# Performance work log

Hardware: AMD Instinct MI355X
Metric: run time of the kernel (lower is better)

## Reference

```python
import jax, jax.numpy as jnp
import numpy as np

DIM, HEAD_DIM, NUM_HEAD, RP_DIM = 1024, 64, 16, 256
B, N = 2, 4096
EPS_KERNEL = 1e-4


def _orthogonal_projection(nb_rows, nb_cols, rng):
    # gaussian_orthogonal_random_matrix with scaling=0 (performer-pytorch)
    blocks = []
    full = nb_rows // nb_cols
    for _ in range(full):
        q, _ = np.linalg.qr(rng.standard_normal((nb_cols, nb_cols)))
        blocks.append(q.T)
    rem = nb_rows - full * nb_cols
    if rem > 0:
        q, _ = np.linalg.qr(rng.standard_normal((nb_cols, nb_cols)))
        blocks.append(q.T[:rem])
    mat = np.concatenate(blocks, axis=0)
    multiplier = np.linalg.norm(rng.standard_normal((nb_rows, nb_cols)), axis=1)
    return (multiplier[:, None] * mat).astype(np.float32)


def setup_inputs() -> dict:
    key = jax.random.key(0)
    ks = jax.random.split(key, 10)
    s = (1.0 / np.sqrt(DIM)).astype(np.float32)
    inp = {
        'X': jax.random.normal(ks[0], (B, N, DIM), jnp.float32),
        'mask': jnp.ones((B, N), jnp.float32),
        'W_q': jax.random.normal(ks[1], (DIM, DIM), jnp.float32) * s,
        'b_q': jnp.zeros((DIM,), jnp.float32),
        'W_k': jax.random.normal(ks[2], (DIM, DIM), jnp.float32) * s,
        'b_k': jnp.zeros((DIM,), jnp.float32),
        'W_v': jax.random.normal(ks[3], (DIM, DIM), jnp.float32) * s,
        'b_v': jnp.zeros((DIM,), jnp.float32),
        'W_ff': jax.random.normal(ks[4], (DIM, DIM), jnp.float32) * s,
        'b_ff': jnp.zeros((DIM,), jnp.float32),
        'proj': jnp.asarray(_orthogonal_projection(RP_DIM, HEAD_DIM, np.random.default_rng(0))),
    }
    return inp


def _softmax_kernel(data, proj, is_query):
    # FAVOR+ positive random features (performer-pytorch softmax_kernel)
    d = data.shape[-1]
    normalizer = d ** -0.25
    ratio = proj.shape[0] ** -0.5
    data_dash = jnp.einsum('bhnd,jd->bhnj', normalizer * data, proj)
    diag_data = jnp.sum(data * data, axis=-1, keepdims=True) * 0.5 * (normalizer ** 2)
    if is_query:
        m = jnp.max(data_dash, axis=-1, keepdims=True)
    else:
        m = jnp.max(data_dash, axis=(-1, -2), keepdims=True)
    return ratio * (jnp.exp(data_dash - diag_data - m) + EPS_KERNEL)


def _split_heads(x):
    b, n, _ = x.shape
    return x.reshape(b, n, NUM_HEAD, HEAD_DIM).transpose(0, 2, 1, 3)


def reference(X, mask, W_q, b_q, W_k, b_k, W_v, b_v, W_ff, b_ff, proj):
    Q = _split_heads(X @ W_q.T + b_q)  # [B,H,N,D]
    K = _split_heads(X @ W_k.T + b_k)
    V = _split_heads(X @ W_v.T + b_v)
    scale = HEAD_DIM ** -0.25  # 1/sqrt(sqrt(head_dim)) applied in PerformerAttention.forward
    m = mask[:, None, :, None]
    qp = _softmax_kernel(Q * scale, proj, is_query=True)   # [B,H,N,R]
    kp = _softmax_kernel(K * scale * m, proj, is_query=False)
    Vm = V * m
    # non-causal linear attention
    k_sum = jnp.sum(kp, axis=-2)                                  # [B,H,R]
    D_inv = 1.0 / jnp.einsum('bhnr,bhr->bhn', qp, k_sum)          # [B,H,N]
    context = jnp.einsum('bhnr,bhne->bhre', kp, Vm)               # [B,H,R,D]
    attn = jnp.einsum('bhre,bhnr,bhn->bhne', context, qp, D_inv)  # [B,H,N,D]
    attn = attn.transpose(0, 2, 1, 3).reshape(X.shape[0], X.shape[1], NUM_HEAD * HEAD_DIM)
    return attn @ W_ff.T + b_ff
```

## Files before the change

### kernel.cpp

```cpp
#include <hip/hip_runtime.h>
#include <math.h>

typedef unsigned short u16;
typedef short bf16x8 __attribute__((ext_vector_type(8)));
typedef float f32x4 __attribute__((ext_vector_type(4)));
typedef u16 u16x4 __attribute__((ext_vector_type(4)));

#define RATIO 0.0625f
#define EPSK 1e-4f
#define LOG2E 1.44269504f

__device__ __forceinline__ float bf2f(u16 u) {
  return __uint_as_float(((unsigned)u) << 16);
}
__device__ __forceinline__ u16 f2bf(float f) {
  unsigned x = __float_as_uint(f);
  x = x + 0x7fffu + ((x >> 16) & 1u);
  return (u16)(x >> 16);
}
__device__ __forceinline__ unsigned cvtpk(float a, float b) {
  unsigned d;
  asm("v_cvt_pk_bf16_f32 %0, %1, %2" : "=v"(d) : "v"(a), "v"(b));
  return d;
}

using as1v = __attribute__((address_space(1))) void;
using as3v = __attribute__((address_space(3))) void;
__device__ __forceinline__ void gl_lds16(const void* g, void* l) {
  __builtin_amdgcn_global_load_lds((as1v*)g, (as3v*)l, 16, 0, 0);
}

__global__ __launch_bounds__(256) void cvt_all(
    const float* __restrict__ X, const float* __restrict__ Wq, const float* __restrict__ Wk,
    const float* __restrict__ Wv, const float* __restrict__ Wff, const float* __restrict__ proj,
    u16* __restrict__ Xbf, u16* __restrict__ Wqkv, u16* __restrict__ Wffb, u16* __restrict__ Pbf) {
  long bid = blockIdx.x;
  const float* src;
  u16* dst;
  long off;
  float sc = 1.f;
  if (bid < 8192) { src = X; dst = Xbf; off = bid; }
  else if (bid < 9216) { src = Wq; dst = Wqkv; off = bid - 8192; }
  else if (bid < 10240) { src = Wk; dst = Wqkv + 1048576; off = bid - 9216; }
  else if (bid < 11264) { src = Wv; dst = Wqkv + 2097152; off = bid - 10240; }
  else if (bid < 12288) { src = Wff; dst = Wffb; off = bid - 11264; }
  else { src = proj; dst = Pbf; off = bid - 12288; sc = 0.125f; }
  long i = (off * 256 + threadIdx.x) * 4;
  f32x4 v = *(const f32x4*)(src + i);
  u16x4 o;
#pragma unroll
  for (int j = 0; j < 4; ++j) o[j] = f2bf(v[j] * sc);
  *(u16x4*)(dst + i) = o;
}

template <int EPI, int NB>
__global__ __launch_bounds__(512, 1) void gemmring(
    const u16* __restrict__ A, const u16* __restrict__ Bw,
    const float* __restrict__ bq, const float* __restrict__ bk,
    const float* __restrict__ bv, const float* __restrict__ mask,
    u16* __restrict__ Q, u16* __restrict__ Kb, u16* __restrict__ Vt,
    float* __restrict__ Of, const float* __restrict__ bff) {
  __shared__ __align__(16) u16 lds[3 * 24576];
  const int nt = 16;
  int tid = threadIdx.x;
  int l = tid & 63, w = tid >> 6;
  int wm = w >> 1, wn = w & 1;
  int lo = l & 15, hi = l >> 4;
  int bid = blockIdx.x;
  int swz = (bid & 7) * ((NB * 32) / 8) + (bid >> 3);
  long m0 = (long)(swz / NB) * 256;
  long c0 = (long)(swz % NB) * 128;
  int srow = tid >> 3;
  int sce = ((tid & 7) ^ ((tid >> 3) & 7)) * 8;
  f32x4 acc[4][4] = {};

  auto stageA = [&](int t) {
    u16* ub = (u16*)lds + (t % 3) * 24576;
    long k0 = (long)t * 64;
#pragma unroll
    for (int u = 0; u < 2; ++u)
#pragma unroll
      for (int j = 0; j < 2; ++j) {
        long row = m0 + u * 128 + j * 64 + srow;
        gl_lds16(A + row * 1024 + k0 + sce, ub + u * 8192 + j * 4096 + tid * 8);
      }
  };
  auto stageB = [&](int t) {
    u16* ub = (u16*)lds + (t % 3) * 24576 + 16384;
    long k0 = (long)t * 64;
#pragma unroll
    for (int j = 0; j < 2; ++j) {
      long row = c0 + j * 64 + srow;
      gl_lds16(Bw + row * 1024 + k0 + sce, ub + j * 4096 + tid * 8);
    }
  };

  stageA(0); stageB(0);
  stageA(1); stageB(1);

  int arb = (wm & 1) * 64;
  for (int t = 0; t < nt; ++t) {
    if (t < nt - 1) {
      asm volatile("s_waitcnt vmcnt(6)" ::: "memory");
    } else {
      asm volatile("s_waitcnt vmcnt(0)" ::: "memory");
    }
    __builtin_amdgcn_s_barrier();
    __builtin_amdgcn_sched_barrier(0);
    const u16* Au = (const u16*)lds + (t % 3) * 24576 + (wm >> 1) * 8192;
    const u16* Bu = (const u16*)lds + (t % 3) * 24576 + 16384;
    bf16x8 areg[4][2], breg[4][2];
#pragma unroll
    for (int mf = 0; mf < 4; ++mf) {
      int lrow = arb + mf * 16 + lo;
#pragma unroll
      for (int kk = 0; kk < 2; ++kk)
        areg[mf][kk] = *(const bf16x8*)(Au + lrow * 64 + ((kk * 32 + hi * 8) ^ ((lo & 7) << 3)));
    }
#pragma unroll
    for (int nf = 0; nf < 4; ++nf) {
      int lrow = wn * 64 + nf * 16 + lo;
#pragma unroll
      for (int kk = 0; kk < 2; ++kk)
        breg[nf][kk] = *(const bf16x8*)(Bu + lrow * 64 + ((kk * 32 + hi * 8) ^ ((lo & 7) << 3)));
    }
    if (t + 2 < nt) { stageA(t + 2); stageB(t + 2); }
#pragma unroll
    for (int mf = 0; mf < 4; ++mf)
#pragma unroll
      for (int nf = 0; nf < 4; ++nf)
#pragma unroll
        for (int kk = 0; kk < 2; ++kk)
          acc[mf][nf] = __builtin_amdgcn_mfma_f32_16x16x32_bf16(areg[mf][kk], breg[nf][kk],
                                                                acc[mf][nf], 0, 0, 0);
  }

  long rowb = m0 + wm * 64;
  if (EPI == 0) {
    int wsel = (int)(c0 >> 10);
    long cw = c0 & 1023;
    if (wsel < 2) {
      const float* bias = wsel ? bk : bq;
      u16* O = wsel ? Kb : Q;
#pragma unroll
      for (int mf = 0; mf < 4; ++mf)
#pragma unroll
        for (int nf = 0; nf < 4; ++nf) {
          long col = cw + wn * 64 + nf * 16 + lo;
          float bi = bias[col];
#pragma unroll
          for (int r = 0; r < 4; ++r) {
            long row = rowb + mf * 16 + hi * 4 + r;
            O[row * 1024 + col] = f2bf(acc[mf][nf][r] + bi);
          }
        }
    } else {
#pragma unroll
      for (int mf = 0; mf < 4; ++mf) {
        long t4 = rowb + mf * 16 + hi * 4;
        long b = t4 >> 12;
        long nn = t4 & 4095;
#pragma unroll
        for (int nf = 0; nf < 4; ++nf) {
          long col = cw + wn * 64 + nf * 16 + lo;
          float bi = bv[col];
          long h = col >> 6, e = col & 63;
          u16x4 pk;
#pragma unroll
          for (int r = 0; r < 4; ++r) pk[r] = f2bf((acc[mf][nf][r] + bi) * mask[t4 + r]);
          *(u16x4*)&Vt[((b * 16 + h) * 64 + e) * 4096 + nn] = pk;
        }
      }
    }
  } else {
#pragma unroll
    for (int mf = 0; mf < 4; ++mf)
#pragma unroll
      for (int nf = 0; nf < 4; ++nf) {
        long col = c0 + wn * 64 + nf * 16 + lo;
        float bi = bff[col];
#pragma unroll
        for (int r = 0; r < 4; ++r) {
          long row = rowb + mf * 16 + hi * 4 + r;
          Of[row * 1024 + col] = acc[mf][nf][r] + bi;
        }
      }
  }
}

__global__ __launch_bounds__(512) void kctx(
    const u16* __restrict__ Kg, const u16* __restrict__ Pbf,
    const u16* __restrict__ Vt, const float* __restrict__ mask,
    u16* __restrict__ part, float* __restrict__ part_ks,
    float* __restrict__ part_m, float* __restrict__ part_vs) {
  __shared__ __align__(16) u16 projL[256 * 64];
  __shared__ __align__(16) u16 KL[256 * 64];
  __shared__ __align__(16) u16 VL[64 * 256];
  __shared__ __align__(16) u16 kpL[256 * 64];
  __shared__ float sdiag[256];
  __shared__ float smask[256];
  int tid = threadIdx.x, l = tid & 63, wq = tid >> 6;
  int lo = l & 15, hi = l >> 4;
  int bh = blockIdx.x, ck2 = blockIdx.y;
  int b = bh >> 4, h = bh & 15;
  int rq = wq * 32;
  int rl = l >> 3;
#pragma unroll
  for (int i = 0; i < 4; ++i) {
    int c = i * 8 + wq;
    int row = c * 8 + rl;
    int sc_ = ((l & 7) * 8) ^ ((row & 7) << 3);
    gl_lds16(Pbf + (long)row * 64 + sc_, projL + c * 512);
  }
  bf16x8 ones;
#pragma unroll
  for (int e = 0; e < 8; ++e) ones[e] = (short)0x3F80;
  float Mw = -3.4e38f;
  f32x4 acc2[2][4] = {};
  f32x4 acc_ks[2] = {};
  f32x4 acc_vs[4] = {};
  for (int s = 0; s < 2; ++s) {
    int ck = ck2 * 2 + s;
    long tg0 = (long)b * 4096 + (long)ck * 256;
    if (s) __syncthreads();
#pragma unroll
    for (int i = 0; i < 4; ++i) {
      int c = i * 8 + wq;
      int row = c * 8 + rl;
      int sc_ = ((l & 7) * 8) ^ ((row & 7) << 3);
      gl_lds16(Kg + (tg0 + row) * 1024 + (long)h * 64 + sc_, KL + c * 512);
    }
#pragma unroll
    for (int i = 0; i < 4; ++i) {
      int c = i * 8 + wq;
      int e = 2 * c + (l >> 5);
      int sc_ = ((l & 31) * 8) ^ ((e & 7) << 3);
      gl_lds16(Vt + ((long)bh * 64 + e) * 4096 + (long)ck * 256 + sc_, VL + c * 512);
    }
    asm volatile("s_waitcnt vmcnt(0)" ::: "memory");
    __syncthreads();
    if (tid < 256) {
      float sm = 0.f;
#pragma unroll
      for (int j = 0; j < 8; ++j) {
        bf16x8 v = *(const bf16x8*)(KL + tid * 64 + ((j * 8) ^ ((tid & 7) << 3)));
#pragma unroll
        for (int e = 0; e < 8; ++e) {
          float f = bf2f((u16)v[e]);
          sm += f * f;
        }
      }
      sdiag[tid] = sm * (1.f / 128.f);
      smask[tid] = mask[tg0 + tid];
    }
    __syncthreads();
    for (int sc = 0; sc < 4; ++sc) {
      f32x4 accT[4][2] = {};
#pragma unroll
      for (int kk = 0; kk < 2; ++kk) {
        bf16x8 aK[4], bP[2];
#pragma unroll
        for (int m = 0; m < 4; ++m)
          aK[m] = *(const bf16x8*)(KL + (sc * 64 + m * 16 + lo) * 64 +
                                   ((kk * 32 + hi * 8) ^ ((lo & 7) << 3)));
#pragma unroll
        for (int nf = 0; nf < 2; ++nf)
          bP[nf] = *(const bf16x8*)(projL + (rq + nf * 16 + lo) * 64 +
                                    ((kk * 32 + hi * 8) ^ ((lo & 7) << 3)));
#pragma unroll
        for (int m = 0; m < 4; ++m)
#pragma unroll
          for (int nf = 0; nf < 2; ++nf)
            accT[m][nf] = __builtin_amdgcn_mfma_f32_16x16x32_bf16(aK[m], bP[nf], accT[m][nf], 0, 0, 0);
      }
      float mloc = -3.4e38f;
#pragma unroll
      for (int m = 0; m < 4; ++m) {
        int tb = m * 16 + hi * 4;
#pragma unroll
        for (int r = 0; r < 4; ++r) {
          float mv = smask[sc * 64 + tb + r];
#pragma unroll
          for (int nf = 0; nf < 2; ++nf) mloc = fmaxf(mloc, mv * accT[m][nf][r]);
        }
      }
#pragma unroll
      for (int sft = 1; sft < 64; sft <<= 1) mloc = fmaxf(mloc, __shfl_xor(mloc, sft, 64));
      float nM = fmaxf(Mw, mloc);
      float rs = __builtin_exp2f((Mw - nM) * LOG2E);
#pragma unroll
      for (int m = 0; m < 2; ++m)
#pragma unroll
        for (int q = 0; q < 4; ++q) {
          acc_ks[m][q] *= rs;
#pragma unroll
          for (int nf = 0; nf < 4; ++nf) acc2[m][nf][q] *= rs;
        }
      Mw = nM;
#pragma unroll
      for (int m = 0; m < 4; ++m) {
        int tb = m * 16 + hi * 4;
        float mv[4], dg[4];
#pragma unroll
        for (int r = 0; r < 4; ++r) {
          int tk = sc * 64 + tb + r;
          mv[r] = smask[tk];
          dg[r] = sdiag[tk];
        }
#pragma unroll
        for (int nf = 0; nf < 2; ++nf) {
          int rr = rq + nf * 16 + lo;
          float v[4];
#pragma unroll
          for (int r = 0; r < 4; ++r) {
            float x = mv[r] * accT[m][nf][r] - mv[r] * mv[r] * dg[r] - Mw;
            v[r] = __builtin_exp2f(x * LOG2E);
          }
          uint2 pk;
          pk.x = cvtpk(v[0], v[1]);
          pk.y = cvtpk(v[2], v[3]);
          *(uint2*)(kpL + rr * 64 + (tb ^ ((lo & 7) << 3))) = pk;
        }
      }
#pragma unroll
      for (int kk = 0; kk < 2; ++kk) {
        bf16x8 aC[2], bV[4];
#pragma unroll
        for (int m = 0; m < 2; ++m)
          aC[m] = *(const bf16x8*)(kpL + (rq + m * 16 + lo) * 64 +
                                   ((kk * 32 + hi * 8) ^ ((lo & 7) << 3)));
#pragma unroll
        for (int nf = 0; nf < 4; ++nf)
          bV[nf] = *(const bf16x8*)(VL + (nf * 16 + lo) * 256 +
                                    ((sc * 64 + kk * 32 + hi * 8) ^ ((lo & 7) << 3)));
#pragma unroll
        for (int m = 0; m < 2; ++m) {
          acc_ks[m] = __builtin_amdgcn_mfma_f32_16x16x32_bf16(aC[m], ones, acc_ks[m], 0, 0, 0);
#pragma unroll
          for (int nf = 0; nf < 4; ++nf)
            acc2[m][nf] = __builtin_amdgcn_mfma_f32_16x16x32_bf16(aC[m], bV[nf], acc2[m][nf], 0, 0, 0);
        }
        if (wq == 0) {
#pragma unroll
          for (int nf = 0; nf < 4; ++nf)
            acc_vs[nf] = __builtin_amdgcn_mfma_f32_16x16x32_bf16(ones, bV[nf], acc_vs[nf], 0, 0, 0);
        }
      }
    }
  }
  long pb = ((long)bh * 8 + ck2) * 64;
#pragma unroll
  for (int m = 0; m < 2; ++m) {
    int r0 = rq + m * 16 + hi * 4;
#pragma unroll
    for (int nf = 0; nf < 4; ++nf) {
      int e = nf * 16 + lo;
      uint2 pk;
      pk.x = cvtpk(acc2[m][nf][0], acc2[m][nf][1]);
      pk.y = cvtpk(acc2[m][nf][2], acc2[m][nf][3]);
      *(uint2*)&part[(pb + e) * 256 + r0] = pk;
    }
    if (lo == 0)
      *(f32x4*)&part_ks[((long)bh * 8 + ck2) * 256 + r0] = acc_ks[m];
  }
  if (l == 0) part_m[((long)bh * 8 + ck2) * 8 + wq] = Mw;
  if (wq == 0 && hi == 0) {
#pragma unroll
    for (int nf = 0; nf < 4; ++nf)
      part_vs[((long)bh * 8 + ck2) * 64 + nf * 16 + lo] = acc_vs[nf][0];
  }
}

__global__ __launch_bounds__(256) void ctx_reduce2(
    const u16* __restrict__ part, const float* __restrict__ part_ks,
    const float* __restrict__ part_m, const float* __restrict__ part_vs,
    u16* __restrict__ ctxb) {
  int bid = blockIdx.x;
  int bh = bid / 80, j = bid % 80;
  int r = threadIdx.x;
  const float* pm = part_m + (long)bh * 64;
  float M = -3.4e38f;
#pragma unroll
  for (int i = 0; i < 64; ++i) M = fmaxf(M, pm[i]);
  int wv = r >> 5;
  float out = 0.f;
  if (j < 64) {
    float s = 0.f, sv = 0.f;
#pragma unroll
    for (int c = 0; c < 8; ++c) {
      s += __builtin_exp2f((pm[c * 8 + wv] - M) * LOG2E) *
           bf2f(part[(((long)bh * 8 + c) * 64 + j) * 256 + r]);
      sv += part_vs[((long)bh * 8 + c) * 64 + j];
    }
    out = RATIO * (s + EPSK * sv);
  } else if (j == 64) {
    float s = 0.f;
#pragma unroll
    for (int c = 0; c < 8; ++c)
      s += __builtin_exp2f((pm[c * 8 + wv] - M) * LOG2E) *
           part_ks[((long)bh * 8 + c) * 256 + r];
    out = RATIO * (s + EPSK * 4096.f);
  }
  ctxb[((long)bh * 80 + j) * 256 + r] = f2bf(out);
}

__global__ __launch_bounds__(256) void qattn(
    const u16* __restrict__ Qg, const u16* __restrict__ Pbf,
    const u16* __restrict__ ctxbg, u16* __restrict__ attn) {
  __shared__ __align__(16) u16 L[69632];
  __shared__ float sdiagq[128];
  __shared__ float sredq[4 * 128];
  u16* projL = L;
  u16* CL = L + 16384;
  u16* QL = L + 36864;
  u16* qpL = L + 36864;
  int tid = threadIdx.x, l = tid & 63, wq = tid >> 6;
  int lo = l & 15, hi = l >> 4;
  int bh = blockIdx.x;
  int b = bh >> 4, h = bh & 15;
  long tokb = (long)b * 4096 + (long)blockIdx.y * 128;
  int rq = wq * 64, tq = wq * 32;
#pragma unroll
  for (int i = 0; i < 8; ++i) {
    int c = wq * 8 + i;
    int row = c * 8 + (l >> 3);
    int sc_ = ((l & 7) * 8) ^ ((row & 7) << 3);
    gl_lds16(Pbf + (long)row * 64 + sc_, projL + c * 512);
  }
#pragma unroll
  for (int i = 0; i < 4; ++i) {
    int c = wq * 4 + i;
    int row = c * 8 + (l >> 3);
    int sc_ = ((l & 7) * 8) ^ ((row & 7) << 3);
    gl_lds16(Qg + (tokb + row) * 1024 + (long)h * 64 + sc_, QL + c * 512);
  }
#pragma unroll
  for (int i = 0; i < 10; ++i) {
    int c = wq * 10 + i;
    int j = 2 * c + (l >> 5);
    int sc_ = ((l & 31) * 8) ^ ((j & 7) << 3);
    gl_lds16(ctxbg + ((long)bh * 80 + j) * 256 + sc_, CL + c * 512);
  }
  asm volatile("s_waitcnt vmcnt(0)" ::: "memory");
  __syncthreads();
  if (tid < 128) {
    float s = 0.f;
#pragma unroll
    for (int j = 0; j < 8; ++j) {
      bf16x8 v = *(const bf16x8*)(QL + tid * 64 + ((j * 8) ^ ((tid & 7) << 3)));
#pragma unroll
      for (int e = 0; e < 8; ++e) {
        float f = bf2f((u16)v[e]);
        s += f * f;
      }
    }
    sdiagq[tid] = s * (1.f / 128.f);
  }
  f32x4 acc[4][8];
#pragma unroll
  for (int m = 0; m < 4; ++m)
#pragma unroll
    for (int nf = 0; nf < 8; ++nf) acc[m][nf] = f32x4{0.f, 0.f, 0.f, 0.f};
#pragma unroll
  for (int kk = 0; kk < 2; ++kk) {
    bf16x8 aP[4], bQ[8];
#pragma unroll
    for (int m = 0; m < 4; ++m)
      aP[m] = *(const bf16x8*)(projL + (rq + m * 16 + lo) * 64 +
                               ((kk * 32 + hi * 8) ^ ((lo & 7) << 3)));
#pragma unroll
    for (int nf = 0; nf < 8; ++nf)
      bQ[nf] = *(const bf16x8*)(QL + (nf * 16 + lo) * 64 +
                                ((kk * 32 + hi * 8) ^ ((lo & 7) << 3)));
#pragma unroll
    for (int m = 0; m < 4; ++m)
#pragma unroll
      for (int nf = 0; nf < 8; ++nf)
        acc[m][nf] = __builtin_amdgcn_mfma_f32_16x16x32_bf16(aP[m], bQ[nf], acc[m][nf], 0, 0, 0);
  }
#pragma unroll
  for (int nf = 0; nf < 8; ++nf) {
    float vm = acc[0][nf][0];
#pragma unroll
    for (int m = 0; m < 4; ++m)
#pragma unroll
      for (int r = 0; r < 4; ++r) vm = fmaxf(vm, acc[m][nf][r]);
    vm = fmaxf(vm, __shfl_xor(vm, 16, 64));
    vm = fmaxf(vm, __shfl_xor(vm, 32, 64));
    if (hi == 0) sredq[wq * 128 + nf * 16 + lo] = vm;
  }
  __syncthreads();
#pragma unroll
  for (int nf = 0; nf < 8; ++nf) {
    int tk = nf * 16 + lo;
    float rm = fmaxf(fmaxf(sredq[tk], sredq[128 + tk]),
                     fmaxf(sredq[256 + tk], sredq[384 + tk]));
    float dg = sdiagq[tk];
#pragma unroll
    for (int m = 0; m < 4; ++m) {
      int r0 = rq + m * 16 + hi * 4;
      float v[4];
#pragma unroll
      for (int r = 0; r < 4; ++r) {
        float x = acc[m][nf][r] - dg - rm;
        v[r] = RATIO * (__builtin_exp2f(x * LOG2E) + EPSK);
      }
      uint2 pk;
      pk.x = cvtpk(v[0], v[1]);
      pk.y = cvtpk(v[2], v[3]);
      *(uint2*)(qpL + tk * 256 + (r0 ^ ((lo & 7) << 3))) = pk;
    }
  }
  __syncthreads();
  f32x4 acc2[5][2];
#pragma unroll
  for (int m = 0; m < 5; ++m)
#pragma unroll
    for (int n = 0; n < 2; ++n) acc2[m][n] = f32x4{0.f, 0.f, 0.f, 0.f};
#pragma unroll
  for (int ks = 0; ks < 8; ++ks) {
    bf16x8 aC[5], bQp[2];
#pragma unroll
    for (int m = 0; m < 5; ++m)
      aC[m] = *(const bf16x8*)(CL + (m * 16 + lo) * 256 +
                               ((ks * 32 + hi * 8) ^ ((lo & 7) << 3)));
#pragma unroll
    for (int n = 0; n < 2; ++n)
      bQp[n] = *(const bf16x8*)(qpL + (tq + n * 16 + lo) * 256 +
                                ((ks * 32 + hi * 8) ^ ((lo & 7) << 3)));
#pragma unroll
    for (int m = 0; m < 5; ++m)
#pragma unroll
      for (int n = 0; n < 2; ++n)
        acc2[m][n] = __builtin_amdgcn_mfma_f32_16x16x32_bf16(aC[m], bQp[n], acc2[m][n], 0, 0, 0);
  }
#pragma unroll
  for (int n = 0; n < 2; ++n) {
    float dv = __shfl(acc2[4][n][0], lo, 64);
    float di = 1.f / dv;
    long tok = tokb + tq + n * 16 + lo;
#pragma unroll
    for (int m = 0; m < 4; ++m) {
      int j0 = m * 16 + hi * 4;
      uint2 pk;
      pk.x = cvtpk(acc2[m][n][0] * di, acc2[m][n][1] * di);
      pk.y = cvtpk(acc2[m][n][2] * di, acc2[m][n][3] * di);
      *(uint2*)&attn[tok * 1024 + (long)h * 64 + j0] = pk;
    }
  }
}

extern "C" void kernel_launch(void* const* d_in, const int* in_sizes, int n_in,
                              void* d_out, int out_size, void* d_ws, size_t ws_size,
                              hipStream_t stream) {
  const float* X = (const float*)d_in[0];
  const float* mask = (const float*)d_in[1];
  const float* Wq = (const float*)d_in[2];
  const float* bq = (const float*)d_in[3];
  const float* Wk = (const float*)d_in[4];
  const float* bk = (const float*)d_in[5];
  const float* Wv = (const float*)d_in[6];
  const float* bv = (const float*)d_in[7];
  const float* Wff = (const float*)d_in[8];
  const float* bff = (const float*)d_in[9];
  const float* proj = (const float*)d_in[10];
  float* out = (float*)d_out;

  char* p = (char*)d_ws;
  u16* Xbf = (u16*)p;   p += 16777216;
  u16* Wqkv = (u16*)p;  p += 6291456;
  u16* Wffb = (u16*)p;  p += 2097152;
  u16* Pbf = (u16*)p;   p += 32768;
  u16* Qbf = (u16*)p;   p += 16777216;
  u16* Kbf = (u16*)p;   p += 16777216;
  u16* Vt = (u16*)p;    p += 16777216;
  u16* ctxb = (u16*)p;  p += 1310720;
  u16* part = (u16*)p;      p += 8388608;
  float* part_ks = (float*)p; p += 262144;
  float* part_m = (float*)p;  p += 8192;
  float* part_vs = (float*)p; p += 65536;
  u16* attn = Xbf;

  cvt_all<<<12304, 256, 0, stream>>>(X, Wq, Wk, Wv, Wff, proj, Xbf, Wqkv, Wffb, Pbf);
  gemmring<0, 24><<<768, 512, 0, stream>>>(Xbf, Wqkv, bq, bk, bv, mask, Qbf, Kbf, Vt, nullptr, nullptr);
  kctx<<<dim3(32, 8), 512, 0, stream>>>(Kbf, Pbf, Vt, mask, part, part_ks, part_m, part_vs);
  ctx_reduce2<<<2560, 256, 0, stream>>>(part, part_ks, part_m, part_vs, ctxb);
  qattn<<<dim3(32, 32), 256, 0, stream>>>(Qbf, Pbf, ctxb, attn);
  gemmring<1, 8><<<256, 512, 0, stream>>>(attn, Wffb, nullptr, nullptr, nullptr, nullptr,
                                          nullptr, nullptr, nullptr, out, bff);
}
```

Baseline: 158.6 us.

## Replace QKV projection GEMM with 256x256-tile double-buffered kernel

```diff
diff --git a/kernel.cpp b/kernel.cpp
--- a/kernel.cpp
+++ b/kernel.cpp
@@ -51,6 +51,130 @@
 #pragma unroll
   for (int j = 0; j < 4; ++j) o[j] = f2bf(v[j] * sc);
   *(u16x4*)(dst + i) = o;
+}
+
+template <int NB>
+__global__ __launch_bounds__(512, 2) void gemm256p(
+    const u16* __restrict__ A, const u16* __restrict__ Bw,
+    const float* __restrict__ bq, const float* __restrict__ bk,
+    const float* __restrict__ bv, const float* __restrict__ mask,
+    u16* __restrict__ Q, u16* __restrict__ Kb, u16* __restrict__ Vt) {
+  __shared__ __align__(16) u16 lds[2 * 32768];
+  const int nt = 16;
+  int tid = threadIdx.x;
+  int l = tid & 63, w = tid >> 6;
+  int wm = w >> 2, wn = w & 3;
+  int lo = l & 15, hi = l >> 4;
+  int bid = blockIdx.x;
+  int swz = (bid & 7) * ((NB * 32) / 8) + (bid >> 3);
+  long m0 = (long)(swz / NB) * 256;
+  long c0 = (long)(swz % NB) * 256;
+  f32x4 acc[8][4] = {};
+
+  auto stageU = [&](int t, int kh, int ab) {
+    const u16* src = ab ? Bw : A;
+    long b0 = ab ? c0 : m0;
+    u16* dst = (u16*)lds + (t & 1) * 32768 + ab * 16384 + kh * 8192;
+    long k0 = (long)t * 64 + kh * 32;
+#pragma unroll
+    for (int j = 0; j < 2; ++j) {
+      int blk = w + j * 8;
+      int row = blk * 16 + (l >> 2);
+      int s = l & 3;
+      int g = (s ^ ((row >> 1) & 3)) * 8;
+      gl_lds16(src + (b0 + row) * 1024 + k0 + g, dst + blk * 512 + l * 8);
+    }
+  };
+
+  stageU(0, 0, 0); stageU(0, 0, 1);
+  stageU(0, 1, 0); stageU(0, 1, 1);
+  stageU(1, 0, 0); stageU(1, 0, 1);
+  asm volatile("s_waitcnt vmcnt(8)" ::: "memory");
+  __builtin_amdgcn_s_barrier();
+  __builtin_amdgcn_sched_barrier(0);
+
+  int cg = (lo >> 1) & 3;
+  for (int t = 0; t < nt; ++t) {
+#pragma unroll
+    for (int kh = 0; kh < 2; ++kh) {
+      const u16* Au = (const u16*)lds + (t & 1) * 32768 + kh * 8192;
+      const u16* Bu = (const u16*)lds + (t & 1) * 32768 + 16384 + kh * 8192;
+      bf16x8 areg[8], breg[4];
+#pragma unroll
+      for (int m = 0; m < 8; ++m) {
+        int row = wm * 128 + m * 16 + lo;
+        areg[m] = *(const bf16x8*)(Au + row * 32 + ((hi ^ cg) * 8));
+      }
+#pragma unroll
+      for (int n = 0; n < 4; ++n) {
+        int row = wn * 64 + n * 16 + lo;
+        breg[n] = *(const bf16x8*)(Bu + row * 32 + ((hi ^ cg) * 8));
+      }
+      if (kh == 0) {
+        if (t + 1 < nt) { stageU(t + 1, 1, 0); stageU(t + 1, 1, 1); }
+      } else {
+        if (t + 2 < nt) { stageU(t + 2, 0, 0); stageU(t + 2, 0, 1); }
+      }
+      if (t < 14 || (t == 14 && kh == 0)) {
+        asm volatile("s_waitcnt vmcnt(8)" ::: "memory");
+      } else if (t == 14) {
+        asm volatile("s_waitcnt vmcnt(4)" ::: "memory");
+      } else if (kh == 0) {
+        asm volatile("s_waitcnt vmcnt(0)" ::: "memory");
+      }
+      asm volatile("s_waitcnt lgkmcnt(8)" ::: "memory");
+      __builtin_amdgcn_s_barrier();
+      asm volatile("s_waitcnt lgkmcnt(0)" ::: "memory");
+      __builtin_amdgcn_sched_barrier(0);
+      __builtin_amdgcn_s_setprio(1);
+#pragma unroll
+      for (int m = 0; m < 8; ++m)
+#pragma unroll
+        for (int n = 0; n < 4; ++n)
+          acc[m][n] = __builtin_amdgcn_mfma_f32_16x16x32_bf16(areg[m], breg[n],
+                                                              acc[m][n], 0, 0, 0);
+      __builtin_amdgcn_s_setprio(0);
+      __builtin_amdgcn_s_barrier();
+      __builtin_amdgcn_sched_barrier(0);
+    }
+  }
+
+  long rowb = m0 + wm * 128;
+  int wsel = (int)(c0 >> 10);
+  long cw = (c0 & 1023) + wn * 64;
+  if (wsel < 2) {
+    const float* bias = wsel ? bk : bq;
+    u16* O = wsel ? Kb : Q;
+#pragma unroll
+    for (int mf = 0; mf < 8; ++mf)
+#pragma unroll
+      for (int nf = 0; nf < 4; ++nf) {
+        long col = cw + nf * 16 + lo;
+        float bi = bias[col];
+#pragma unroll
+        for (int r = 0; r < 4; ++r) {
+          long row = rowb + mf * 16 + hi * 4 + r;
+          O[row * 1024 + col] = f2bf(acc[mf][nf][r] + bi);
+        }
+      }
+  } else {
+#pragma unroll
+    for (int mf = 0; mf < 8; ++mf) {
+      long t4 = rowb + mf * 16 + hi * 4;
+      long b = t4 >> 12;
+      long nn = t4 & 4095;
+#pragma unroll
+      for (int nf = 0; nf < 4; ++nf) {
+        long col = cw + nf * 16 + lo;
+        float bi = bv[col];
+        long h = col >> 6, e = col & 63;
+        u16x4 pk;
+#pragma unroll
+        for (int r = 0; r < 4; ++r) pk[r] = f2bf((acc[mf][nf][r] + bi) * mask[t4 + r]);
+        *(u16x4*)&Vt[((b * 16 + h) * 64 + e) * 4096 + nn] = pk;
+      }
+    }
+  }
 }
 
 template <int EPI, int NB>
@@ -582,7 +706,7 @@
   u16* attn = Xbf;
 
   cvt_all<<<12304, 256, 0, stream>>>(X, Wq, Wk, Wv, Wff, proj, Xbf, Wqkv, Wffb, Pbf);
-  gemmring<0, 24><<<768, 512, 0, stream>>>(Xbf, Wqkv, bq, bk, bv, mask, Qbf, Kbf, Vt, nullptr, nullptr);
+  gemm256p<12><<<384, 512, 0, stream>>>(Xbf, Wqkv, bq, bk, bv, mask, Qbf, Kbf, Vt);
   kctx<<<dim3(32, 8), 512, 0, stream>>>(Kbf, Pbf, Vt, mask, part, part_ks, part_m, part_vs);
   ctx_reduce2<<<2560, 256, 0, stream>>>(part, part_ks, part_m, part_vs, ctxb);
   qattn<<<dim3(32, 32), 256, 0, stream>>>(Qbf, Pbf, ctxb, attn);
```

After: 175.1 us. +10.5%, slower.
